# Performance work log

Hardware: AMD Instinct MI355X
Metric: run time of the kernel (lower is better)

## Reference

```python
import jax, jax.numpy as jnp
import numpy as np

FEATURE_W = 1.0
TRIPLET_W = 1.0
SOFT_W = 1.0
MARGIN = 0.2
TEMP = 1.0
COMMIT_W = 0.1
DISTORT_W = 0.1
STRIDE = 320

B, T, D, K = 8, 1500, 512, 4096


def setup_inputs() -> dict:
    key = jax.random.key(0)
    k1, k2, k3, k4, k5 = jax.random.split(key, 5)
    return {
        "student_features": jax.random.normal(k1, (B, T, D), dtype=jnp.float32),
        "teacher_features": jax.random.normal(k2, (B, T, D), dtype=jnp.float32),
        "teacher_codes": jax.random.randint(k3, (B, T), 0, K),
        "codebook": jax.random.normal(k4, (K, D), dtype=jnp.float32),
        "lengths": jax.random.randint(k5, (B,), 0, T * STRIDE),
    }


def _sq_dists(flat, codebook):
    x2 = jnp.sum(flat * flat, axis=-1, keepdims=True)          # (N,1)
    c2 = jnp.sum(codebook * codebook, axis=-1)[None, :]        # (1,K)
    xc = jnp.einsum("nd,kd->nk", flat, codebook)               # (N,K)
    return jnp.maximum(x2 + c2 - 2.0 * xc, 0.0)


def reference(student_features, teacher_features, teacher_codes, codebook, lengths):
    b, t, d = student_features.shape
    # valid-frame mask from sample lengths
    valid = jnp.minimum(lengths // STRIDE, t)                  # (B,)
    mask = (jnp.arange(t)[None, :] < valid[:, None]).astype(student_features.dtype)  # (B,T)
    msum = jnp.sum(mask)

    # feature loss: masked mean of per-token MSE
    diff = student_features - teacher_features
    feature_loss = jnp.sum(jnp.mean(diff * diff, axis=-1) * mask) / msum

    # triplet loss
    pos_dist = jnp.sqrt(jnp.sum(diff * diff, axis=-1))
    neg_teacher = jnp.roll(teacher_features, shift=1, axis=0)
    nd = student_features - neg_teacher
    neg_dist = jnp.sqrt(jnp.sum(nd * nd, axis=-1))
    triplet = jax.nn.relu(pos_dist - neg_dist + MARGIN)
    triplet_loss = jnp.sum(triplet * mask) / msum

    # soft token (KL distillation over codebook logits)
    s_flat = student_features.reshape(-1, d)                   # (B*T, D)
    t_flat = teacher_features.reshape(-1, d)
    s_logits = -_sq_dists(s_flat, codebook) / TEMP             # (B*T, K)
    t_logits = -_sq_dists(t_flat, codebook) / TEMP
    s_logp = jax.nn.log_softmax(s_logits, axis=-1)
    t_logp = jax.nn.log_softmax(t_logits, axis=-1)
    t_prob = jax.lax.stop_gradient(jnp.exp(t_logp))
    t_logp = jax.lax.stop_gradient(t_logp)
    kl_per_token = jnp.sum(t_prob * (t_logp - s_logp), axis=-1)  # (B*T,)
    flat_mask = mask.reshape(-1)
    soft_loss = jnp.sum(kl_per_token * flat_mask) / msum

    # VQ commitment / distortion (nearest-code quantization)
    codes = jnp.argmax(s_logits, axis=-1)                       # argmin dist == argmax logits
    quantized = codebook[codes].reshape(b, t, d)
    cdiff = student_features - jax.lax.stop_gradient(quantized)
    commitment_loss = jnp.mean(cdiff * cdiff)
    ddiff = jax.lax.stop_gradient(student_features) - quantized
    distortion_loss = jnp.mean(ddiff * ddiff)

    total = (FEATURE_W * feature_loss + TRIPLET_W * triplet_loss
             + SOFT_W * soft_loss + COMMIT_W * commitment_loss
             + DISTORT_W * distortion_loss)
    return total
```

## Files before the change

### kernel.cpp

```cpp
#include <hip/hip_runtime.h>

typedef unsigned short u16;
typedef unsigned int   u32;
typedef float  f32x16 __attribute__((ext_vector_type(16)));
typedef __bf16 bf16x8 __attribute__((ext_vector_type(8)));

#define B_N   8
#define T_N   1500
#define D_N   512
#define K_N   4096
#define NTOK  12000
#define STRD  320

#define X2S_OFF     0u
#define C2_OFF      49152u
#define FEATP_OFF   65536u
#define TRIPP_OFF   67584u
#define STATEP_OFF  69632u
#define SBF_OFF     1048576u
#define TBF_OFF     (1048576u + 12288000u)
#define CBBF_OFF    (1048576u + 24576000u)

#define ST_S1  12000
#define ST_SQ  48000


__device__ __forceinline__ u16 f2bf(float x){
  u32 u = __float_as_uint(x);
  u32 r = (u + 0x7fffu + ((u >> 16) & 1u)) >> 16;
  return (u16)r;
}

__device__ __forceinline__ void gl_lds16(const void* g, void* l){
  __builtin_amdgcn_global_load_lds(
      (__attribute__((address_space(1))) void*)(g),
      (__attribute__((address_space(3))) void*)(l),
      16, 0, 0);
}

__device__ __forceinline__ void merge_state(float& m, float& Z, float om, float oZ){
  float nm = fmaxf(m, om);
  Z = Z*__expf(m - nm) + oZ*__expf(om - nm);
  m = nm;
}
__device__ __forceinline__ void merge_stateT(float& m, float& Z, float& A,
                                             float om, float oZ, float oA){
  float nm = fmaxf(m, om);
  float e0 = __expf(m - nm), e1 = __expf(om - nm);
  Z = Z*e0 + oZ*e1; A = A*e0 + oA*e1; m = nm;
}

__global__ __launch_bounds__(256) void prep_kernel(
    const float* __restrict__ s, const float* __restrict__ t,
    const float* __restrict__ cb, const int* __restrict__ lengths,
    u16* __restrict__ sbf, u16* __restrict__ tbf, u16* __restrict__ cbbf,
    float* __restrict__ x2s, float* __restrict__ c2,
    float* __restrict__ featP, float* __restrict__ tripP)
{
  const int tid = threadIdx.x;
  const int w = tid >> 6, lane = tid & 63;
  __shared__ float sred[3][32];

  if (blockIdx.x < 375){
    const int tt = blockIdx.x;
    const int t8 = lane >> 3, kpart = lane & 7;
    const int tokL = w*8 + t8;
    const int n = tt*32 + tokL;
    const int b = n / T_N, tok = n - b*T_N;
    const int nr = ((b+7)&7)*T_N + tok;
    const float* srow = s + (size_t)n  * D_N;
    const float* trow = t + (size_t)n  * D_N;
    const float* rrow = t + (size_t)nr * D_N;

    float x2 = 0.f, sd2 = 0.f, nd2 = 0.f;
    uint4 sbq[8], tbq[8];
#pragma unroll
    for (int q = 0; q < 8; ++q){
      const int kl = q*64 + kpart*8;
      float4 a0 = *(const float4*)(srow + kl), a1 = *(const float4*)(srow + kl + 4);
      float4 b0 = *(const float4*)(trow + kl), b1 = *(const float4*)(trow + kl + 4);
      float4 r0 = *(const float4*)(rrow + kl), r1 = *(const float4*)(rrow + kl + 4);
      float sv[8] = {a0.x,a0.y,a0.z,a0.w,a1.x,a1.y,a1.z,a1.w};
      float tv[8] = {b0.x,b0.y,b0.z,b0.w,b1.x,b1.y,b1.z,b1.w};
      float rv[8] = {r0.x,r0.y,r0.z,r0.w,r1.x,r1.y,r1.z,r1.w};
      u16 sb[8], tb[8];
#pragma unroll
      for (int i = 0; i < 8; ++i){
        float d = sv[i] - tv[i]; sd2 += d*d;
        x2 += sv[i]*sv[i];
        float e = sv[i] - rv[i]; nd2 += e*e;
        sb[i] = f2bf(sv[i]); tb[i] = f2bf(tv[i]);
      }
      sbq[q].x = (u32)sb[0] | ((u32)sb[1]<<16); sbq[q].y = (u32)sb[2] | ((u32)sb[3]<<16);
      sbq[q].z = (u32)sb[4] | ((u32)sb[5]<<16); sbq[q].w = (u32)sb[6] | ((u32)sb[7]<<16);
      tbq[q].x = (u32)tb[0] | ((u32)tb[1]<<16); tbq[q].y = (u32)tb[2] | ((u32)tb[3]<<16);
      tbq[q].z = (u32)tb[4] | ((u32)tb[5]<<16); tbq[q].w = (u32)tb[6] | ((u32)tb[7]<<16);
    }
#pragma unroll
    for (int q = 0; q < 8; ++q){
      const int ks = q*4 + (kpart >> 1), kh = kpart & 1;
      const size_t chunk = ((size_t)tt*32 + ks)*64 + kh*32 + tokL;
      ((uint4*)sbf)[chunk] = sbq[q];
      ((uint4*)tbf)[chunk] = tbq[q];
    }
#pragma unroll
    for (int mm = 1; mm < 8; mm <<= 1){
      x2  += __shfl_xor(x2,  mm);
      sd2 += __shfl_xor(sd2, mm);
      nd2 += __shfl_xor(nd2, mm);
    }
    if (kpart == 0){ sred[0][tokL] = x2; sred[1][tokL] = sd2; sred[2][tokL] = nd2; }
    __syncthreads();
    if (tid < 32){
      float X2 = sred[0][tid], SD = sred[1][tid], ND = sred[2][tid];
      int n2 = tt*32 + tid, b2 = n2 / T_N, tk2 = n2 - b2*T_N;
      x2s[n2] = X2;
      int valid = lengths[b2] / STRD; if (valid > T_N) valid = T_N;
      float mf = (tk2 < valid) ? 1.f : 0.f;
      float fp = mf * SD * (1.f/512.f);
      float tp = mf * fmaxf(sqrtf(SD) - sqrtf(ND) + 0.2f, 0.f);
#pragma unroll
      for (int mm = 1; mm < 32; mm <<= 1){ fp += __shfl_xor(fp, mm); tp += __shfl_xor(tp, mm); }
      if (tid == 0){ featP[tt] = fp; tripP[tt] = tp; }
    }
  } else {
    const int idx = blockIdx.x - 375;
    const int ctile = idx*4 + w;
    const int kh = lane >> 5, sp = lane & 31;
    const int ch = ctile >> 5, cg = (ctile >> 3) & 3, ctg = ctile & 7;
    const int code = ctile*32 + sp;
    const float* crow = cb + (size_t)code * D_N;

    float s2 = 0.f;
#pragma unroll
    for (int stp = 0; stp < 32; ++stp){
      const int kc = stp >> 1, ks2 = stp & 1;
      const int k0 = stp*16 + kh*8;
      float4 c0 = *(const float4*)(crow + k0), c1 = *(const float4*)(crow + k0 + 4);
      float cv[8] = {c0.x,c0.y,c0.z,c0.w,c1.x,c1.y,c1.z,c1.w};
      u16 cbv[8];
#pragma unroll
      for (int i = 0; i < 8; ++i){ s2 += cv[i]*cv[i]; cbv[i] = f2bf(cv[i]); }
      uint4 pk;
      pk.x = (u32)cbv[0] | ((u32)cbv[1]<<16); pk.y = (u32)cbv[2] | ((u32)cbv[3]<<16);
      pk.z = (u32)cbv[4] | ((u32)cbv[5]<<16); pk.w = (u32)cbv[6] | ((u32)cbv[7]<<16);
      const size_t off = ((size_t)(ch*64 + cg*16 + kc))*8192 + ctg*1024 + ks2*512 + lane*8;
      *(uint4*)(cbbf + off) = pk;
    }
    s2 += __shfl_xor(s2, 32);
    if (lane < 32) c2[ctile*32 + lane] = s2;
  }
}

__global__ __launch_bounds__(256, 3) void main_kl_kernel(
    const u16* __restrict__ sbf, const u16* __restrict__ tbf,
    const u16* __restrict__ cbbf, const float* __restrict__ c2,
    float* __restrict__ stateP)
{
  __shared__ u16 Ab[2][2048];

  const int tid = threadIdx.x;
  const int w = tid >> 6, lane = tid & 63;
  const int kh = lane >> 5;
  const int blk = blockIdx.x;
  const int tt = blk % 375, ch = blk / 375;

  const u16* cbB = cbbf + (size_t)ch * 524288;
  const int mat = tid >> 7, inner = tid & 127;
  const u16* aSrc = (mat ? tbf : sbf) + (size_t)tt*16384;

  gl_lds16(aSrc + ((size_t)(inner >> 6)*64 + (inner & 63))*8,
           &Ab[0][mat*1024 + inner*8]);
  bf16x8 b00, b01, b10, b11;
  {
    const u16* rg = cbB;
    b00 = *(const bf16x8*)(rg + (w*2+0)*1024 +       lane*8);
    b01 = *(const bf16x8*)(rg + (w*2+0)*1024 + 512 + lane*8);
    b10 = *(const bf16x8*)(rg + (w*2+1)*1024 +       lane*8);
    b11 = *(const bf16x8*)(rg + (w*2+1)*1024 + 512 + lane*8);
  }

  float mS = -3e38f, zS = 0.f, mT = -3e38f, zT = 0.f, aa = 0.f;
  f32x16 a0s, a0t, a1s, a1t;

  for (int c = 0; c < 64; ++c){
    const int kc = c & 15, p = c & 1;
    if (kc == 0){
#pragma unroll
      for (int i = 0; i < 16; ++i){ a0s[i]=0.f; a0t[i]=0.f; a1s[i]=0.f; a1t[i]=0.f; }
    }
    __syncthreads();
    if (c < 63){
      const int kc1 = (c+1) & 15;
      gl_lds16(aSrc + (((size_t)kc1*2 + (inner >> 6))*64 + (inner & 63))*8,
               &Ab[p^1][mat*1024 + inner*8]);
    }
    bf16x8 n00 = b00, n01 = b01, n10 = b10, n11 = b11;
    if (c < 63){
      const u16* rg = cbB + (size_t)(c+1)*8192;
      n00 = *(const bf16x8*)(rg + (w*2+0)*1024 +       lane*8);
      n01 = *(const bf16x8*)(rg + (w*2+0)*1024 + 512 + lane*8);
      n10 = *(const bf16x8*)(rg + (w*2+1)*1024 +       lane*8);
      n11 = *(const bf16x8*)(rg + (w*2+1)*1024 + 512 + lane*8);
    }

    const u16* ap = &Ab[p][0];
    bf16x8 as0 = *(const bf16x8*)(ap +        lane*8);
    bf16x8 at0 = *(const bf16x8*)(ap + 1024 + lane*8);
    bf16x8 as1 = *(const bf16x8*)(ap +  512 + lane*8);
    bf16x8 at1 = *(const bf16x8*)(ap + 1536 + lane*8);
    a0s = __builtin_amdgcn_mfma_f32_32x32x16_bf16(b00, as0, a0s, 0, 0, 0);
    a0t = __builtin_amdgcn_mfma_f32_32x32x16_bf16(b00, at0, a0t, 0, 0, 0);
    a1s = __builtin_amdgcn_mfma_f32_32x32x16_bf16(b10, as0, a1s, 0, 0, 0);
    a1t = __builtin_amdgcn_mfma_f32_32x32x16_bf16(b10, at0, a1t, 0, 0, 0);
    a0s = __builtin_amdgcn_mfma_f32_32x32x16_bf16(b01, as1, a0s, 0, 0, 0);
    a0t = __builtin_amdgcn_mfma_f32_32x32x16_bf16(b01, at1, a0t, 0, 0, 0);
    a1s = __builtin_amdgcn_mfma_f32_32x32x16_bf16(b11, as1, a1s, 0, 0, 0);
    a1t = __builtin_amdgcn_mfma_f32_32x32x16_bf16(b11, at1, a1t, 0, 0, 0);
    b00 = n00; b01 = n01; b10 = n10; b11 = n11;

    if (kc == 15){
      const int cg = c >> 4;
#pragma unroll
      for (int ct = 0; ct < 2; ++ct){
        const f32x16& vS = ct ? a1s : a0s;
        const f32x16& vT = ct ? a1t : a0t;
        const int ctg = w*2 + ct;
        const float* c2b = c2 + ch*1024 + cg*256 + ctg*32 + kh*4;
        float4 g0 = *(const float4*)(c2b);
        float4 g1 = *(const float4*)(c2b + 8);
        float4 g2 = *(const float4*)(c2b + 16);
        float4 g3 = *(const float4*)(c2b + 24);
        float c2v[16] = {g0.x,g0.y,g0.z,g0.w, g1.x,g1.y,g1.z,g1.w,
                         g2.x,g2.y,g2.z,g2.w, g3.x,g3.y,g3.z,g3.w};
        float ms_t = -3e38f, mt_t = -3e38f;
#pragma unroll
        for (int i = 0; i < 16; ++i){
          ms_t = fmaxf(ms_t, 2.0f*vS[i] - c2v[i]);
          mt_t = fmaxf(mt_t, 2.0f*vT[i] - c2v[i]);
        }
        float nmS = fmaxf(mS, ms_t), nmT = fmaxf(mT, mt_t);
        float esS = __expf(mS - nmS), esT = __expf(mT - nmT);
        zS *= esS; zT *= esT; aa *= esT;
#pragma unroll
        for (int i = 0; i < 16; ++i){
          float sl = 2.0f*vS[i] - c2v[i];
          float tl = 2.0f*vT[i] - c2v[i];
          zS += __expf(sl - nmS);
          float e = __expf(tl - nmT);
          zT += e; aa += e*(tl - sl);
        }
        mS = nmS; mT = nmT;
      }
    }
  }

  {
    float om = __shfl_xor(mS, 32), oZ = __shfl_xor(zS, 32);
    merge_state(mS, zS, om, oZ);
    float omt = __shfl_xor(mT, 32), ozt = __shfl_xor(zT, 32), oA = __shfl_xor(aa, 32);
    merge_stateT(mT, zT, aa, omt, ozt, oA);
  }
  __syncthreads();
  float* wst = (float*)&Ab[0][0];
  if (lane < 32){
    float* pw = wst + (w*32 + lane)*5;
    pw[0] = mS; pw[1] = zS; pw[2] = mT; pw[3] = zT; pw[4] = aa;
  }
  __syncthreads();
  if (tid < 32){
    const float* p0 = wst + tid*5;
    float m_s = p0[0], z_s = p0[1], m_t = p0[2], z_t = p0[3], a = p0[4];
#pragma unroll
    for (int ww = 1; ww < 4; ++ww){
      const float* pw = wst + (ww*32 + tid)*5;
      merge_state(m_s, z_s, pw[0], pw[1]);
      merge_stateT(m_t, z_t, a, pw[2], pw[3], pw[4]);
    }
    const int n = tt*32 + tid;
    stateP[0*ST_SQ + ch*ST_S1 + n] = m_s;
    stateP[1*ST_SQ + ch*ST_S1 + n] = z_s;
    stateP[2*ST_SQ + ch*ST_S1 + n] = m_t;
    stateP[3*ST_SQ + ch*ST_S1 + n] = z_t;
    stateP[4*ST_SQ + ch*ST_S1 + n] = a;
  }
}

__global__ __launch_bounds__(1024) void tail_kernel(
    const float* __restrict__ stateP, const float* __restrict__ x2s,
    const float* __restrict__ featP, const float* __restrict__ tripP,
    const int* __restrict__ lengths, float* __restrict__ out)
{
  const int tid = threadIdx.x;
  double kl_s = 0.0, md_s = 0.0, f = 0.0, tr = 0.0;
  for (int n = tid; n < NTOK; n += 1024){
    float m_s = stateP[0*ST_SQ + n], z_s = stateP[1*ST_SQ + n];
    float m_t = stateP[2*ST_SQ + n], z_t = stateP[3*ST_SQ + n], a = stateP[4*ST_SQ + n];
#pragma unroll
    for (int chh = 1; chh < 4; ++chh){
      merge_state(m_s, z_s, stateP[0*ST_SQ + chh*ST_S1 + n], stateP[1*ST_SQ + chh*ST_S1 + n]);
      merge_stateT(m_t, z_t, a, stateP[2*ST_SQ + chh*ST_S1 + n],
                   stateP[3*ST_SQ + chh*ST_S1 + n], stateP[4*ST_SQ + chh*ST_S1 + n]);
    }
    float klv = a / z_t - (m_t + __logf(z_t)) + (m_s + __logf(z_s));
    int b = n / T_N, tk = n - b*T_N;
    int valid = lengths[b] / STRD; if (valid > T_N) valid = T_N;
    if (tk < valid) kl_s += (double)klv;
    md_s += (double)fmaxf(x2s[n] - m_s, 0.f);
  }
  for (int i = tid; i < 375; i += 1024){ f += (double)featP[i]; tr += (double)tripP[i]; }
#pragma unroll
  for (int mm = 1; mm < 64; mm <<= 1){
    kl_s += __shfl_xor(kl_s, mm); md_s += __shfl_xor(md_s, mm);
    f    += __shfl_xor(f,    mm); tr   += __shfl_xor(tr,   mm);
  }
  __shared__ double red[16][4];
  const int w = tid >> 6, lane = tid & 63;
  if (lane == 0){ red[w][0]=kl_s; red[w][1]=md_s; red[w][2]=f; red[w][3]=tr; }
  __syncthreads();
  if (tid == 0){
    double KL=0, MD=0, F=0, TR=0;
    for (int ww = 0; ww < 16; ++ww){ KL+=red[ww][0]; MD+=red[ww][1]; F+=red[ww][2]; TR+=red[ww][3]; }
    long msum = 0;
    for (int b = 0; b < 8; ++b){ int v = lengths[b] / STRD; if (v > T_N) v = T_N; msum += v; }
    double inv = 1.0 / (double)msum;
    double total = F*inv + TR*inv + KL*inv + 0.2 * MD / ((double)B_N * T_N * D_N);
    out[0] = (float)total;
  }
}

extern "C" void kernel_launch(void* const* d_in, const int* in_sizes, int n_in,
                              void* d_out, int out_size, void* d_ws, size_t ws_size,
                              hipStream_t stream)
{
  const float* s  = (const float*)d_in[0];
  const float* t  = (const float*)d_in[1];
  const float* cb = (const float*)d_in[3];
  const int* lengths = (const int*)d_in[4];

  char* ws = (char*)d_ws;
  float* x2s    = (float*)(ws + X2S_OFF);
  float* c2     = (float*)(ws + C2_OFF);
  float* featP  = (float*)(ws + FEATP_OFF);
  float* tripP  = (float*)(ws + TRIPP_OFF);
  float* stateP = (float*)(ws + STATEP_OFF);
  u16* sbf  = (u16*)(ws + SBF_OFF);
  u16* tbf  = (u16*)(ws + TBF_OFF);
  u16* cbbf = (u16*)(ws + CBBF_OFF);

  prep_kernel<<<407, 256, 0, stream>>>(s, t, cb, lengths, sbf, tbf, cbbf,
                                       x2s, c2, featP, tripP);
  main_kl_kernel<<<1500, 256, 0, stream>>>(sbf, tbf, cbbf, c2, stateP);
  tail_kernel<<<1, 1024, 0, stream>>>(stateP, x2s, featP, tripP, lengths, (float*)d_out);
}
```

Baseline: 246.8 us.

## Stage full student/teacher token tile in LDS once, drop per-step barriers

```diff
diff --git a/kernel.cpp b/kernel.cpp
--- a/kernel.cpp
+++ b/kernel.cpp
@@ -152,12 +152,12 @@
   }
 }
 
-__global__ __launch_bounds__(256, 3) void main_kl_kernel(
+__global__ __launch_bounds__(256, 2) void main_kl_kernel(
     const u16* __restrict__ sbf, const u16* __restrict__ tbf,
     const u16* __restrict__ cbbf, const float* __restrict__ c2,
     float* __restrict__ stateP)
 {
-  __shared__ u16 Ab[2][2048];
+  __shared__ u16 Ab[32768];
 
   const int tid = threadIdx.x;
   const int w = tid >> 6, lane = tid & 63;
@@ -166,11 +166,16 @@
   const int tt = blk % 375, ch = blk / 375;
 
   const u16* cbB = cbbf + (size_t)ch * 524288;
-  const int mat = tid >> 7, inner = tid & 127;
-  const u16* aSrc = (mat ? tbf : sbf) + (size_t)tt*16384;
-
-  gl_lds16(aSrc + ((size_t)(inner >> 6)*64 + (inner & 63))*8,
-           &Ab[0][mat*1024 + inner*8]);
+  const u16* sA = sbf + (size_t)tt * 16384;
+  const u16* tA = tbf + (size_t)tt * 16384;
+
+#pragma unroll
+  for (int r = 0; r < 8; ++r){
+    const int off = (r*256 + tid)*8;
+    gl_lds16(sA + off, &Ab[off]);
+    gl_lds16(tA + off, &Ab[16384 + off]);
+  }
+
   bf16x8 b00, b01, b10, b11;
   {
     const u16* rg = cbB;
@@ -180,20 +185,16 @@
     b11 = *(const bf16x8*)(rg + (w*2+1)*1024 + 512 + lane*8);
   }
 
+  __syncthreads();
+
   float mS = -3e38f, zS = 0.f, mT = -3e38f, zT = 0.f, aa = 0.f;
   f32x16 a0s, a0t, a1s, a1t;
 
   for (int c = 0; c < 64; ++c){
-    const int kc = c & 15, p = c & 1;
+    const int kc = c & 15;
     if (kc == 0){
 #pragma unroll
       for (int i = 0; i < 16; ++i){ a0s[i]=0.f; a0t[i]=0.f; a1s[i]=0.f; a1t[i]=0.f; }
-    }
-    __syncthreads();
-    if (c < 63){
-      const int kc1 = (c+1) & 15;
-      gl_lds16(aSrc + (((size_t)kc1*2 + (inner >> 6))*64 + (inner & 63))*8,
-               &Ab[p^1][mat*1024 + inner*8]);
     }
     bf16x8 n00 = b00, n01 = b01, n10 = b10, n11 = b11;
     if (c < 63){
@@ -204,11 +205,12 @@
       n11 = *(const bf16x8*)(rg + (w*2+1)*1024 + 512 + lane*8);
     }
 
-    const u16* ap = &Ab[p][0];
-    bf16x8 as0 = *(const bf16x8*)(ap +        lane*8);
-    bf16x8 at0 = *(const bf16x8*)(ap + 1024 + lane*8);
-    bf16x8 as1 = *(const bf16x8*)(ap +  512 + lane*8);
-    bf16x8 at1 = *(const bf16x8*)(ap + 1536 + lane*8);
+    const u16* ap = &Ab[kc*1024 + lane*8];
+    bf16x8 as0 = *(const bf16x8*)(ap);
+    bf16x8 as1 = *(const bf16x8*)(ap + 512);
+    bf16x8 at0 = *(const bf16x8*)(ap + 16384);
+    bf16x8 at1 = *(const bf16x8*)(ap + 16896);
+
     a0s = __builtin_amdgcn_mfma_f32_32x32x16_bf16(b00, as0, a0s, 0, 0, 0);
     a0t = __builtin_amdgcn_mfma_f32_32x32x16_bf16(b00, at0, a0t, 0, 0, 0);
     a1s = __builtin_amdgcn_mfma_f32_32x32x16_bf16(b10, as0, a1s, 0, 0, 0);
@@ -262,7 +264,7 @@
     merge_stateT(mT, zT, aa, omt, ozt, oA);
   }
   __syncthreads();
-  float* wst = (float*)&Ab[0][0];
+  float* wst = (float*)&Ab[0];
   if (lane < 32){
     float* pw = wst + (w*32 + lane)*5;
     pw[0] = mS; pw[1] = zS; pw[2] = mT; pw[3] = zT; pw[4] = aa;
```

Result: faster. 237.1 us (median of 3 runs) (-3.9%).
